# Performance work log

Hardware: AMD Instinct MI355X
Metric: run time of the kernel (lower is better)

The kernel has to match this reference:

```python
import jax, jax.numpy as jnp
import numpy as np
import math

N_HEADS = 8
N_LAYERS = 2
HYPER1 = 0.6
HYPER2 = 0.07


def setup_inputs() -> dict:
    key = jax.random.key(0)
    ks = jax.random.split(key, 32)
    B, S, D, M = 32, 512, 768, 384  # M = mem_dim = D // 2
    rn = lambda k, shape, scale: jax.random.normal(k, shape, jnp.float32) * scale
    sd, sm = 1.0 / math.sqrt(D), 1.0 / math.sqrt(M)
    inp = {
        'gcn_inputs': rn(ks[0], (B, S, D), 1.0),
        'adj_matrix': jax.random.uniform(ks[1], (B, S, S), jnp.float32),
        'attn_mask': jax.random.randint(ks[2], (B, 1, S), 0, 2).astype(jnp.int32),
        's_mask': jax.random.randint(ks[3], (B, S), 0, 2).astype(jnp.int32),
        'a_mask': jax.random.randint(ks[4], (B, S), 0, 2).astype(jnp.int32),
        # MultiHeadAttention: two Linear(d_model, d_model) for q and k
        'Wq': rn(ks[5], (D, D), sd), 'bq': jnp.zeros((D,), jnp.float32),
        'Wk': rn(ks[6], (D, D), sd), 'bk': jnp.zeros((D,), jnp.float32),
        # semW / depW: layer0 D->M, layer1 M->M
        'semW0': rn(ks[7], (D, M), sd), 'semb0': jnp.zeros((M,), jnp.float32),
        'semW1': rn(ks[8], (M, M), sm), 'semb1': jnp.zeros((M,), jnp.float32),
        'depW0': rn(ks[9], (D, M), sd), 'depb0': jnp.zeros((M,), jnp.float32),
        'depW1': rn(ks[10], (M, M), sm), 'depb1': jnp.zeros((M,), jnp.float32),
        # projection head fc1: M->32, fc2: 32->M
        'fc1W': rn(ks[11], (M, 32), sm), 'fc1b': jnp.zeros((32,), jnp.float32),
        'fc2W': rn(ks[12], (32, M), 1.0 / math.sqrt(32)), 'fc2b': jnp.zeros((M,), jnp.float32),
        # fc3: M->M, fc4: D->M
        'fc3W': rn(ks[13], (M, M), sm), 'fc3b': jnp.zeros((M,), jnp.float32),
        'fc4W': rn(ks[14], (D, M), sd), 'fc4b': jnp.zeros((M,), jnp.float32),
    }
    return inp


def _sim(z1, z2):
    # F.normalize(dim=2) then bmm
    n1 = z1 / jnp.maximum(jnp.linalg.norm(z1, axis=2, keepdims=True), 1e-12)
    n2 = z2 / jnp.maximum(jnp.linalg.norm(z2, axis=2, keepdims=True), 1e-12)
    return jnp.einsum('bsd,btd->bst', n1, n2)


def _diag(m):
    return jnp.diagonal(m, axis1=-2, axis2=-1)


def _scope_semi_loss(z1, z2, sm, am):
    f = lambda x: jnp.exp(x / HYPER2)
    a_z1 = z1 * am[..., None]
    m_between = f(_sim(a_z1, z2))
    m_refl = f(_sim(a_z1, z1))
    s_z1 = z1 * sm[..., None]
    s_z2 = z2 * sm[..., None]
    as_refl = f(_sim(a_z1, s_z1))
    as_between = f(_sim(a_z1, s_z2))
    w = _sim(a_z1, s_z2)
    weighted = f(w * _diag(w)[..., None])
    pos = (_diag(as_between)
           + (as_refl.sum(2) - _diag(as_refl))
           + (weighted.sum(2) - _diag(weighted)))
    alle = m_refl.sum(2) + m_between.sum(2) - _diag(m_refl)
    return -jnp.log(pos / alle)


def reference(gcn_inputs, adj_matrix, attn_mask, s_mask, a_mask,
              Wq, bq, Wk, bk,
              semW0, semb0, semW1, semb1,
              depW0, depb0, depW1, depb1,
              fc1W, fc1b, fc2W, fc2b, fc3W, fc3b, fc4W, fc4b):
    B, S, D = gcn_inputs.shape
    h, dk = N_HEADS, D // N_HEADS

    # ---- MultiHeadAttention -> per-head attention adjacency ----
    q = (gcn_inputs @ Wq + bq).reshape(B, S, h, dk).transpose(0, 2, 1, 3)
    k = (gcn_inputs @ Wk + bk).reshape(B, S, h, dk).transpose(0, 2, 1, 3)
    scores = jnp.einsum('bhsd,bhtd->bhst', q, k) / math.sqrt(dk)
    scores = jnp.where(attn_mask[:, None] == 0, -10000.0, scores)  # [B,1,1,S] broadcast
    attn = jax.nn.softmax(scores, axis=-1)  # dropout in eval mode -> identity

    # average heads, zero diagonal, add identity, row-mask by encoder atts
    adj_ag = attn.mean(axis=1)  # [B,S,S]
    eye = jnp.eye(S, dtype=adj_ag.dtype)
    adj_ag = adj_ag * (1.0 - eye) + eye
    atts = attn_mask.astype(adj_ag.dtype)  # text_encoder_atts [B,1,S]
    adj_ag = jnp.swapaxes(atts, 1, 2) * adj_ag

    # ---- gated dual-GCN layers ----
    sem_params = [(semW0, semb0), (semW1, semb1)]
    dep_params = [(depW0, depb0), (depW1, depb1)]
    H_l = gcn_inputs
    I_sem = None
    for l in range(N_LAYERS):
        sW, sb = sem_params[l]
        dW, db = dep_params[l]
        AH_sem = jnp.einsum('bst,btd->bsd', adj_ag, H_l)
        I_sem = AH_sem @ sW + sb
        AH_dep = jnp.einsum('bst,btd->bsd', adj_matrix, H_l)
        I_dep = AH_dep @ dW + db
        g = jax.nn.sigmoid(I_dep)
        I_dep_g = HYPER1 * g
        I_com = (1.0 - I_dep_g) * I_sem + I_dep_g * I_dep
        H_out = jax.nn.relu(I_com @ fc3W + fc3b)
        if l == 0:
            H_l = H_l @ fc4W + fc4b
        g_l = jax.nn.sigmoid(H_l)
        H_l = g_l * H_out + (1.0 - g_l) * H_l

    # ---- projection + symmetric contrastive scope loss ----
    proj = lambda z: jax.nn.elu(z @ fc1W + fc1b) @ fc2W + fc2b
    h1 = proj(H_l)
    h2 = proj(I_sem)
    smf = s_mask.astype(h1.dtype)
    amf = a_mask.astype(h1.dtype)
    l1 = _scope_semi_loss(h1, h2, smf, amf)
    l2 = _scope_semi_loss(h2, h1, smf, amf)
    loss = (l1 + l2) * 0.5
    loss_cl = loss.mean(axis=1, keepdims=True).mean()
    return loss_cl
```

## Files before the change

kernel.cpp:

```cpp
#include <hip/hip_runtime.h>
#include <math.h>


typedef __bf16 bf16x8 __attribute__((ext_vector_type(8)));
typedef __bf16 bf16x4 __attribute__((ext_vector_type(4)));
typedef float f32x4 __attribute__((ext_vector_type(4)));

__device__ __forceinline__ void glds16(const void* g, void* l) {
    __builtin_amdgcn_global_load_lds(
        (const __attribute__((address_space(1))) unsigned*)g,
        (__attribute__((address_space(3))) unsigned*)l, 16, 0, 0);
}

__device__ __forceinline__ float sigf(float x) { return 1.f / (1.f + __expf(-x)); }

__global__ __launch_bounds__(256) void mfma_gemm(
    const __bf16* __restrict__ A, const __bf16* __restrict__ B,
    const float* __restrict__ bias, int bzDiv, int bzStride,
    const __bf16* __restrict__ E,
    float* __restrict__ Cf, __bf16* __restrict__ Cb,
    int K, int lda, int ldb, int ldc, int nMax,
    long sAo, long sAi, long sBo, long sBi, int zInner, long sC, int act)
{
    __shared__ __bf16 As[2][128 * 32];
    __shared__ __bf16 Bs[2][128 * 32];
    int z = blockIdx.z;
    long aBase = (long)(z / zInner) * sAo + (long)(z % zInner) * sAi;
    long bBase = (long)(z / zInner) * sBo + (long)(z % zInner) * sBi;
    long cBase = (long)z * sC;
    int m0 = blockIdx.x * 128, n0 = blockIdx.y * 128;
    int tid = threadIdx.x;
    int wave = tid >> 6, lane = tid & 63;
    int wm = wave >> 1, wn = wave & 1;

    int e0 = tid, e1 = tid + 256;
    const __bf16* Ag0 = A + aBase + (long)(m0 + (e0 >> 2)) * lda + (e0 & 3) * 8;
    const __bf16* Ag1 = A + aBase + (long)(m0 + (e1 >> 2)) * lda + (e1 & 3) * 8;
    const __bf16* Bg0 = B + bBase + (long)(n0 + (e0 >> 2)) * ldb + (e0 & 3) * 8;
    const __bf16* Bg1 = B + bBase + (long)(n0 + (e1 >> 2)) * ldb + (e1 & 3) * 8;

    f32x4 acc[4][4];
#pragma unroll
    for (int i = 0; i < 4; i++)
#pragma unroll
        for (int j = 0; j < 4; j++) acc[i][j] = (f32x4){0.f, 0.f, 0.f, 0.f};

    int arow = wm * 64 + (lane & 15);
    int brow = wn * 64 + (lane & 15);
    int quad = lane >> 4;

    glds16(Ag0, As[0] + e0 * 8); glds16(Ag1, As[0] + e1 * 8);
    glds16(Bg0, Bs[0] + e0 * 8); glds16(Bg1, Bs[0] + e1 * 8);

    int cur = 0;
    for (int k0 = 0; k0 < K; k0 += 32) {
        __syncthreads();
        if (k0 + 32 < K) {
            int nk = k0 + 32, nb = cur ^ 1;
            glds16(Ag0 + nk, As[nb] + e0 * 8); glds16(Ag1 + nk, As[nb] + e1 * 8);
            glds16(Bg0 + nk, Bs[nb] + e0 * 8); glds16(Bg1 + nk, Bs[nb] + e1 * 8);
        }
        const bf16x8* Asv = (const bf16x8*)As[cur];
        const bf16x8* Bsv = (const bf16x8*)Bs[cur];
        bf16x8 af[4], bfr[4];
#pragma unroll
        for (int mi = 0; mi < 4; mi++) af[mi] = Asv[(arow + mi * 16) * 4 + quad];
#pragma unroll
        for (int ni = 0; ni < 4; ni++) bfr[ni] = Bsv[(brow + ni * 16) * 4 + quad];
#pragma unroll
        for (int mi = 0; mi < 4; mi++)
#pragma unroll
            for (int ni = 0; ni < 4; ni++)
                acc[mi][ni] = __builtin_amdgcn_mfma_f32_16x16x32_bf16(
                    af[mi], bfr[ni], acc[mi][ni], 0, 0, 0);
        cur ^= 1;
    }

    int crow = m0 + wm * 64 + (lane >> 4) * 4;
    int ccol = n0 + wn * 64 + (lane & 15);
    const float* biasz = bias ? bias + (z / bzDiv) * bzStride : nullptr;
    float bv[4];
#pragma unroll
    for (int ni = 0; ni < 4; ni++) {
        int col = ccol + ni * 16;
        bv[ni] = (biasz && col < nMax) ? biasz[col] : 0.f;
    }
#pragma unroll
    for (int mi = 0; mi < 4; mi++) {
#pragma unroll
        for (int ni = 0; ni < 4; ni++) {
            int col = ccol + ni * 16;
            if (col >= nMax) continue;
#pragma unroll
            for (int r = 0; r < 4; r++) {
                float v = acc[mi][ni][r] + bv[ni];
                long idx = cBase + (long)(crow + mi * 16 + r) * ldc + col;
                if (act == 1) v = fmaxf(v, 0.f);
                else if (act == 2) v = (v > 0.f) ? v : expm1f(v);
                else if (act == 4) {
                    float e = (float)E[idx];
                    v = fmaxf(v, 0.f);
                    float g = sigf(e);
                    v = g * v + (1.f - g) * e;
                }
                if (Cf) Cf[idx] = v;
                if (Cb) Cb[idx] = (__bf16)v;
            }
        }
    }
}

struct WCast {
    const float* src[10];
    unsigned dstOff[10];
    int R[10], C[10];
    int start[11];
};

__global__ __launch_bounds__(256) void castW_kernel(WCast wc, __bf16* wb)
{
    __shared__ float t[32][33];
    int bid = blockIdx.x;
    int e = 0;
    while (bid >= wc.start[e + 1]) e++;
    int tt = bid - wc.start[e];
    int cT = wc.C[e] >> 5;
    int ty = tt / cT, tx = tt - ty * cT;
    const float* in = wc.src[e];
    __bf16* out = wb + wc.dstOff[e];
    int R = wc.R[e], C = wc.C[e];
    int r0 = ty * 32, c0 = tx * 32;
    int tid = threadIdx.x;
    int r = tid >> 3, c4 = (tid & 7) * 4;
    float4 v = *(const float4*)(in + (long)(r0 + r) * C + c0 + c4);
    t[r][c4] = v.x; t[r][c4 + 1] = v.y; t[r][c4 + 2] = v.z; t[r][c4 + 3] = v.w;
    __syncthreads();
    int c = tid >> 3, r4 = (tid & 7) * 4;
    bf16x4 o;
    o[0] = (__bf16)t[r4 + 0][c]; o[1] = (__bf16)t[r4 + 1][c];
    o[2] = (__bf16)t[r4 + 2][c]; o[3] = (__bf16)t[r4 + 3][c];
    *(bf16x4*)(out + (long)(c0 + c) * R + r0 + r4) = o;
}

__global__ void cast_bf16_kernel(const float* __restrict__ in, __bf16* __restrict__ out, long n4)
{
    long i = (long)blockIdx.x * blockDim.x + threadIdx.x;
    if (i < n4) {
        float4 v = ((const float4*)in)[i];
        bf16x4 o; o[0] = (__bf16)v.x; o[1] = (__bf16)v.y; o[2] = (__bf16)v.z; o[3] = (__bf16)v.w;
        ((bf16x4*)out)[i] = o;
    }
}

__global__ __launch_bounds__(256) void softmax_combine(
    const __bf16* __restrict__ scores, const int* __restrict__ attn_mask,
    __bf16* __restrict__ adj_agb, int b0)
{
    const int S = 512;
    int s = blockIdx.x, bl = blockIdx.y, b = b0 + bl;
    int tid = threadIdx.x;
    const float scale = 0.1020620726159658f;
    int t0 = tid, t1 = tid + 256;
    int cm0 = attn_mask[b * S + t0], cm1 = attn_mask[b * S + t1];
    float vals[8][2], part[8];
#pragma unroll
    for (int h = 0; h < 8; ++h) {
        long rb = ((long)(bl * 8 + h) * S + s) * S;
        float r0 = (float)scores[rb + t0], r1 = (float)scores[rb + t1];
        vals[h][0] = cm0 ? __expf(r0 * scale) : 0.f;
        vals[h][1] = cm1 ? __expf(r1 * scale) : 0.f;
        part[h] = vals[h][0] + vals[h][1];
    }
    __shared__ float red[4][8];
    __shared__ float linv[8];
    int lane = tid & 63, w = tid >> 6;
#pragma unroll
    for (int h = 0; h < 8; ++h) {
        float v = part[h];
        for (int o = 32; o > 0; o >>= 1) v += __shfl_down(v, o);
        if (lane == 0) red[w][h] = v;
    }
    __syncthreads();
    if (tid < 8) {
        float l = red[0][tid] + red[1][tid] + red[2][tid] + red[3][tid];
        linv[tid] = 1.f / fmaxf(l, 1e-30f);
    }
    __syncthreads();
    float rowmask = attn_mask[b * S + s] ? 1.f : 0.f;
    float a0 = 0.f, a1 = 0.f;
#pragma unroll
    for (int h = 0; h < 8; ++h) { a0 += vals[h][0] * linv[h]; a1 += vals[h][1] * linv[h]; }
    a0 *= 0.125f; a1 *= 0.125f;
    if (t0 == s) a0 = 1.f;
    if (t1 == s) a1 = 1.f;
    long ob = ((long)b * S + s) * S;
    adj_agb[ob + t0] = (__bf16)(rowmask * a0);
    adj_agb[ob + t1] = (__bf16)(rowmask * a1);
}

__global__ void gcn_combine2(const __bf16* __restrict__ IsIdb,
                             __bf16* __restrict__ Icomb, long n8)
{
    long i = (long)blockIdx.x * blockDim.x + threadIdx.x;
    if (i >= n8) return;
    bf16x8 sv = ((const bf16x8*)IsIdb)[i];
    bf16x8 dv = ((const bf16x8*)(IsIdb + n8 * 8))[i];
    bf16x8 o;
#pragma unroll
    for (int j = 0; j < 8; j++) {
        float s = (float)sv[j], d = (float)dv[j];
        float g = 0.6f * sigf(d);
        o[j] = (__bf16)((1.f - g) * s + g * d);
    }
    ((bf16x8*)Icomb)[i] = o;
}

__global__ __launch_bounds__(128) void rownorm(__bf16* __restrict__ hb, int Dm)
{
    __bf16* p = hb + (long)blockIdx.x * Dm;
    int tid = threadIdx.x;
    float ss = 0.f;
    for (int i = tid; i < Dm; i += 128) { float v = (float)p[i]; ss += v * v; }
    for (int o = 32; o > 0; o >>= 1) ss += __shfl_down(ss, o);
    __shared__ float sb[2];
    __shared__ float scale;
    if ((tid & 63) == 0) sb[tid >> 6] = ss;
    __syncthreads();
    if (tid == 0) scale = 1.f / fmaxf(sqrtf(sb[0] + sb[1]), 1e-12f);
    __syncthreads();
    for (int i = tid; i < Dm; i += 128) p[i] = (__bf16)((float)p[i] * scale);
}

__global__ __launch_bounds__(256) void loss_kernel(
    const __bf16* __restrict__ G11, const __bf16* __restrict__ G12,
    const __bf16* __restrict__ G22,
    const int* __restrict__ s_mask, const int* __restrict__ a_mask,
    float* __restrict__ lossb)
{
    const int S = 512;
    int s = blockIdx.x, b = blockIdx.y;
    int tid = threadIdx.x;
    if (a_mask[b * S + s] == 0) {
        if (tid == 0) lossb[b * S + s] = 0.f;
        return;
    }
    long base = ((long)b * S + s) * S;
    long cbase = (long)b * S * S + s;
    const float it = 1.f / 0.07f;
    float sms = s_mask[b * S + s] ? 1.f : 0.f;
    float d12 = (float)G12[base + s];
    float w1i = sms * d12 * it, w2i = w1i;
    float p[8];
#pragma unroll
    for (int h = 0; h < 8; h++) p[h] = 0.f;
#pragma unroll
    for (int j = 0; j < 2; j++) {
        int t = tid + j * 256;
        bool smt = s_mask[b * S + t] != 0;
        bool off = (t != s);
        float g11 = (float)G11[base + t], g12 = (float)G12[base + t];
        float g21 = (float)G12[cbase + (long)t * S];
        float g22 = (float)G22[base + t];
        float e11 = __expf(g11 * it), e12 = __expf(g12 * it);
        float e21 = __expf(g21 * it), e22 = __expf(g22 * it);
        p[2] += e11; p[3] += e12; p[6] += e22; p[7] += e21;
        if (off) {
            p[0] += smt ? e11 : 1.f;
            p[4] += smt ? e22 : 1.f;
            p[1] += smt ? __expf(g12 * w1i) : 1.f;
            p[5] += smt ? __expf(g21 * w2i) : 1.f;
        }
    }
    __shared__ float red[4][8];
    int lane = tid & 63, w = tid >> 6;
#pragma unroll
    for (int h = 0; h < 8; h++) {
        float v = p[h];
        for (int o = 32; o > 0; o >>= 1) v += __shfl_down(v, o);
        if (lane == 0) red[w][h] = v;
    }
    __syncthreads();
    if (tid == 0) {
        float r[8];
#pragma unroll
        for (int h = 0; h < 8; h++) r[h] = red[0][h] + red[1][h] + red[2][h] + red[3][h];
        float g11ss = (float)G11[base + s], g22ss = (float)G22[base + s];
        float pos1 = __expf(w1i) + r[0] + r[1];
        float alle1 = r[2] - __expf(g11ss * it) + r[3];
        float pos2 = __expf(w2i) + r[4] + r[5];
        float alle2 = r[6] - __expf(g22ss * it) + r[7];
        lossb[b * S + s] = 0.5f * ((__logf(alle1) - __logf(pos1)) +
                                   (__logf(alle2) - __logf(pos2)));
    }
}

__global__ __launch_bounds__(256) void final_reduce(
    const float* __restrict__ lossb, float* __restrict__ out, int n)
{
    int tid = threadIdx.x;
    float s = 0.f;
    for (int i = tid; i < n; i += 256) s += lossb[i];
    for (int o = 32; o > 0; o >>= 1) s += __shfl_down(s, o);
    __shared__ float sb[4];
    if ((tid & 63) == 0) sb[tid >> 6] = s;
    __syncthreads();
    if (tid == 0) out[0] = (sb[0] + sb[1] + sb[2] + sb[3]) / (float)n;
}

static inline void mg(hipStream_t st, const __bf16* A, const __bf16* B,
                      const float* bias, int bzDiv, int bzStride,
                      const __bf16* E, float* Cf, __bf16* Cb,
                      int M, int Npad, int nMax, int K, int lda, int ldb, int ldc,
                      long sAo, long sAi, long sBo, long sBi, int zInner, long sC, int nz,
                      int act)
{
    dim3 g(M / 128, Npad / 128, nz);
    mfma_gemm<<<g, 256, 0, st>>>(A, B, bias, bzDiv, bzStride, E, Cf, Cb,
                                 K, lda, ldb, ldc, nMax,
                                 sAo, sAi, sBo, sBi, zInner, sC, act);
}

extern "C" void kernel_launch(void* const* d_in, const int* in_sizes, int n_in,
                              void* d_out, int out_size, void* d_ws, size_t ws_size,
                              hipStream_t stream)
{
    const int B = 32, S = 512, D = 768, Mm = 384;
    const int MT = B * S;
    const float* X    = (const float*)d_in[0];
    const float* adjm = (const float*)d_in[1];
    const int* attn_mask = (const int*)d_in[2];
    const int* s_mask    = (const int*)d_in[3];
    const int* a_mask    = (const int*)d_in[4];
    const float* Wq = (const float*)d_in[5],  *bq = (const float*)d_in[6];
    const float* Wk = (const float*)d_in[7],  *bk = (const float*)d_in[8];
    const float* semW0 = (const float*)d_in[9],  *semb0 = (const float*)d_in[10];
    const float* semW1 = (const float*)d_in[11], *semb1 = (const float*)d_in[12];
    const float* depW0 = (const float*)d_in[13], *depb0 = (const float*)d_in[14];
    const float* depW1 = (const float*)d_in[15], *depb1 = (const float*)d_in[16];
    const float* fc1W = (const float*)d_in[17], *fc1b = (const float*)d_in[18];
    const float* fc2W = (const float*)d_in[19], *fc2b = (const float*)d_in[20];
    const float* fc3W = (const float*)d_in[21], *fc3b = (const float*)d_in[22];
    const float* fc4W = (const float*)d_in[23], *fc4b = (const float*)d_in[24];

    char* ws = (char*)d_ws;
    const size_t MB = 1u << 20;
    const size_t KB = 1u << 10;

    __bf16* Xb      = (__bf16*)(ws + 0 * MB);
    __bf16* adj_agb = (__bf16*)(ws + 24 * MB);
    __bf16* adjmb   = (__bf16*)(ws + 40 * MB);
    __bf16* qkb     = (__bf16*)(ws + 56 * MB);
    __bf16* scoreB  = (__bf16*)(ws + 104 * MB);
    __bf16* P64     = (__bf16*)(ws + 56 * MB);
    __bf16* IsIdb   = (__bf16*)(ws + 80 * MB);
    __bf16* Isemb   = IsIdb;
    __bf16* Icomb   = (__bf16*)(ws + 104 * MB);
    __bf16* Hpreb   = (__bf16*)(ws + 116 * MB);
    __bf16* Hb      = (__bf16*)(ws + 128 * MB);
    __bf16* t1b     = (__bf16*)(ws + 0 * MB);
    __bf16* hb12    = (__bf16*)(ws + 140 * MB);
    __bf16* h1b     = hb12;
    __bf16* h2b     = hb12 + (long)MT * Mm;
    __bf16* G11     = (__bf16*)(ws + 24 * MB);
    __bf16* G12     = (__bf16*)(ws + 40 * MB);
    __bf16* G22     = (__bf16*)(ws + 72 * MB);

    char* wreg = ws + 192 * MB;
    __bf16* wb     = (__bf16*)wreg;
    __bf16* WqkT   = (__bf16*)(wreg + 0 * KB);
    __bf16* semW0T = (__bf16*)(wreg + 2304 * KB);
    __bf16* depW0T = (__bf16*)(wreg + 2880 * KB);
    __bf16* fc4WT  = (__bf16*)(wreg + 3456 * KB);
    __bf16* semW1T = (__bf16*)(wreg + 4032 * KB);
    __bf16* depW1T = (__bf16*)(wreg + 4320 * KB);
    __bf16* fc3WT  = (__bf16*)(wreg + 4608 * KB);
    __bf16* fc1WT  = (__bf16*)(wreg + 4896 * KB);
    __bf16* fc2WT  = (__bf16*)(wreg + 4992 * KB);
    float*  bqk    = (float*)(wreg + 5016 * KB);
    float*  sbd0   = (float*)(wreg + 5024 * KB);
    float*  sbd1   = (float*)(wreg + 5028 * KB);
    float*  lossb  = (float*)(wreg + 5036 * KB);

    long nSM = (long)S * Mm, nSS = (long)S * S;
    long nPM = (long)Mm * S;

    cast_bf16_kernel<<<(MT * D / 4 + 255) / 256, 256, 0, stream>>>(X, Xb, (long)MT * D / 4);
    cast_bf16_kernel<<<((long)B * nSS / 4 + 255) / 256, 256, 0, stream>>>(adjm, adjmb, (long)B * nSS / 4);
    {
        WCast wc;
        const float* srcs[10] = {Wq, Wk, semW0, depW0, fc4W, semW1, depW1, fc3W, fc1W, fc2W};
        unsigned offs[10] = {0u, 589824u, 1179648u, 1474560u, 1769472u,
                             2064384u, 2211840u, 2359296u, 2506752u, 2555904u};
        int Rs[10] = {768, 768, 768, 768, 768, 384, 384, 384, 384, 32};
        int Cs[10] = {768, 768, 384, 384, 384, 384, 384, 384, 32, 384};
        int st = 0;
        for (int i = 0; i < 10; i++) {
            wc.src[i] = srcs[i]; wc.dstOff[i] = offs[i];
            wc.R[i] = Rs[i]; wc.C[i] = Cs[i];
            wc.start[i] = st; st += (Rs[i] / 32) * (Cs[i] / 32);
        }
        wc.start[10] = st;
        castW_kernel<<<st, 256, 0, stream>>>(wc, wb);
    }
    hipMemsetAsync(fc1WT + 32 * Mm, 0, (size_t)96 * Mm * 2, stream);
    hipMemcpyAsync(bqk, bq, D * 4, hipMemcpyDeviceToDevice, stream);
    hipMemcpyAsync(bqk + D, bk, D * 4, hipMemcpyDeviceToDevice, stream);
    hipMemcpyAsync(sbd0, semb0, Mm * 4, hipMemcpyDeviceToDevice, stream);
    hipMemcpyAsync(sbd0 + Mm, depb0, Mm * 4, hipMemcpyDeviceToDevice, stream);
    hipMemcpyAsync(sbd1, semb1, Mm * 4, hipMemcpyDeviceToDevice, stream);
    hipMemcpyAsync(sbd1 + Mm, depb1, Mm * 4, hipMemcpyDeviceToDevice, stream);

    mg(stream, Xb, WqkT, bqk, 1, 0, nullptr, nullptr, qkb, MT, 1536, 1536, D,
       D, D, 1536, 0, 0, 0, 0, 1, 0, 1, 0);

    for (int c = 0; c < 2; c++) {
        const __bf16* qc = qkb + (long)c * 16 * S * 1536;
        mg(stream, qc, qc + 768, nullptr, 1, 0, nullptr, nullptr, scoreB, S, S, S, 96,
           1536, 1536, S, (long)S * 1536, 96, (long)S * 1536, 96, 8, nSS, 128, 0);
        softmax_combine<<<dim3(S, 16), 256, 0, stream>>>(scoreB, attn_mask, adj_agb, c * 16);
    }

    long n8 = (long)MT * Mm / 8;
    int cwg = (int)((n8 + 255) / 256);

    mg(stream, semW0T, Xb, nullptr, 1, 0, nullptr, nullptr, P64, Mm, S, S, D,
       D, D, S, (long)Mm * D, 0, 0, (long)S * D, 32, nPM, 64, 0);
    mg(stream, adj_agb, P64, sbd0, 32, Mm, nullptr, nullptr, IsIdb, S, Mm, Mm, S,
       S, S, Mm, 0, nSS, 0, nPM, 64, nSM, 64, 0);
    gcn_combine2<<<cwg, 256, 0, stream>>>(IsIdb, Icomb, n8);
    mg(stream, Xb, fc4WT, fc4b, 1, 0, nullptr, nullptr, Hpreb, MT, Mm, Mm, D,
       D, D, Mm, 0, 0, 0, 0, 1, 0, 1, 0);
    mg(stream, Icomb, fc3WT, fc3b, 1, 0, Hpreb, nullptr, Hb, MT, Mm, Mm, Mm,
       Mm, Mm, Mm, 0, 0, 0, 0, 1, 0, 1, 4);

    mg(stream, semW1T, Hb, nullptr, 1, 0, nullptr, nullptr, P64, Mm, S, S, Mm,
       Mm, Mm, S, (long)Mm * Mm, 0, 0, nSM, 32, nPM, 64, 0);
    mg(stream, adj_agb, P64, sbd1, 32, Mm, nullptr, nullptr, IsIdb, S, Mm, Mm, S,
       S, S, Mm, 0, nSS, 0, nPM, 64, nSM, 64, 0);
    gcn_combine2<<<cwg, 256, 0, stream>>>(IsIdb, Icomb, n8);
    mg(stream, Icomb, fc3WT, fc3b, 1, 0, Hb, nullptr, Hb, MT, Mm, Mm, Mm,
       Mm, Mm, Mm, 0, 0, 0, 0, 1, 0, 1, 4);

    long sAproj = (long)(Isemb - Hb);
    mg(stream, Hb, fc1WT, fc1b, 1, 0, nullptr, nullptr, t1b, MT, 128, 32, Mm,
       Mm, Mm, 32, 0, sAproj, 0, 0, 2, (long)MT * 32, 2, 2);
    mg(stream, t1b, fc2WT, fc2b, 1, 0, nullptr, nullptr, hb12, MT, Mm, Mm, 32,
       32, 32, Mm, 0, (long)MT * 32, 0, 0, 2, (long)MT * Mm, 2, 0);

    rownorm<<<2 * MT, 128, 0, stream>>>(hb12, Mm);

    mg(stream, h1b, h1b, nullptr, 1, 0, nullptr, nullptr, G11, S, S, S, Mm,
       Mm, Mm, S, 0, nSM, 32 * nSM, nSM, 32, nSS, 64, 0);
    mg(stream, h2b, h2b, nullptr, 1, 0, nullptr, nullptr, G22, S, S, S, Mm,
       Mm, Mm, S, 0, nSM, 0, nSM, 32, nSS, 32, 0);

    loss_kernel<<<dim3(S, B), 256, 0, stream>>>(G11, G12, G22, s_mask, a_mask, lossb);
    final_reduce<<<1, 256, 0, stream>>>(lossb, (float*)d_out, MT);
}
```

Before: 793.4 us.

## Fuse fc4 into QK GEMM and gate combine into dep adjacency GEMM

The fc4 projection is folded into the Q/K projection GEMM by widening the weight matrix to 1920 columns, so X is read once and one launch is removed. The fc3 epilogue then reads its residual from a strided slice of that output. The separate gcn_combine2 kernel is removed: the sem and dep adjacency GEMMs are now split, and the dep GEMM applies the sigmoid gate in its epilogue (act 5) against the stored sem result. This saves a full pass over the intermediate, at the cost of a wider QK buffer and two smaller batched GEMM launches instead of one.

```diff
diff --git a/kernel.cpp b/kernel.cpp
--- a/kernel.cpp
+++ b/kernel.cpp
@@ -17,7 +17,7 @@
 __global__ __launch_bounds__(256) void mfma_gemm(
     const __bf16* __restrict__ A, const __bf16* __restrict__ B,
     const float* __restrict__ bias, int bzDiv, int bzStride,
-    const __bf16* __restrict__ E,
+    const __bf16* __restrict__ E, long ldE, long sCE,
     float* __restrict__ Cf, __bf16* __restrict__ Cb,
     int K, int lda, int ldb, int ldc, int nMax,
     long sAo, long sAi, long sBo, long sBi, int zInner, long sC, int act)
@@ -94,14 +94,19 @@
 #pragma unroll
             for (int r = 0; r < 4; r++) {
                 float v = acc[mi][ni][r] + bv[ni];
-                long idx = cBase + (long)(crow + mi * 16 + r) * ldc + col;
+                int row = crow + mi * 16 + r;
+                long idx = cBase + (long)row * ldc + col;
                 if (act == 1) v = fmaxf(v, 0.f);
                 else if (act == 2) v = (v > 0.f) ? v : expm1f(v);
                 else if (act == 4) {
-                    float e = (float)E[idx];
+                    float e = (float)E[(long)z * sCE + (long)row * ldE + col];
                     v = fmaxf(v, 0.f);
                     float g = sigf(e);
                     v = g * v + (1.f - g) * e;
+                } else if (act == 5) {
+                    float s = (float)E[(long)z * sCE + (long)row * ldE + col];
+                    float g = 0.6f * sigf(v);
+                    v = (1.f - g) * s + g * v;
                 }
                 if (Cf) Cf[idx] = v;
                 if (Cb) Cb[idx] = (__bf16)v;
@@ -196,23 +201,6 @@
     long ob = ((long)b * S + s) * S;
     adj_agb[ob + t0] = (__bf16)(rowmask * a0);
     adj_agb[ob + t1] = (__bf16)(rowmask * a1);
-}
-
-__global__ void gcn_combine2(const __bf16* __restrict__ IsIdb,
-                             __bf16* __restrict__ Icomb, long n8)
-{
-    long i = (long)blockIdx.x * blockDim.x + threadIdx.x;
-    if (i >= n8) return;
-    bf16x8 sv = ((const bf16x8*)IsIdb)[i];
-    bf16x8 dv = ((const bf16x8*)(IsIdb + n8 * 8))[i];
-    bf16x8 o;
-#pragma unroll
-    for (int j = 0; j < 8; j++) {
-        float s = (float)sv[j], d = (float)dv[j];
-        float g = 0.6f * sigf(d);
-        o[j] = (__bf16)((1.f - g) * s + g * d);
-    }
-    ((bf16x8*)Icomb)[i] = o;
 }
 
 __global__ __launch_bounds__(128) void rownorm(__bf16* __restrict__ hb, int Dm)
@@ -309,13 +297,14 @@
 
 static inline void mg(hipStream_t st, const __bf16* A, const __bf16* B,
                       const float* bias, int bzDiv, int bzStride,
-                      const __bf16* E, float* Cf, __bf16* Cb,
+                      const __bf16* E, long ldE, long sCE,
+                      float* Cf, __bf16* Cb,
                       int M, int Npad, int nMax, int K, int lda, int ldb, int ldc,
                       long sAo, long sAi, long sBo, long sBi, int zInner, long sC, int nz,
                       int act)
 {
     dim3 g(M / 128, Npad / 128, nz);
-    mfma_gemm<<<g, 256, 0, st>>>(A, B, bias, bzDiv, bzStride, E, Cf, Cb,
+    mfma_gemm<<<g, 256, 0, st>>>(A, B, bias, bzDiv, bzStride, E, ldE, sCE, Cf, Cb,
                                  K, lda, ldb, ldc, nMax,
                                  sAo, sAi, sBo, sBi, zInner, sC, act);
 }
@@ -350,45 +339,45 @@
     __bf16* adj_agb = (__bf16*)(ws + 24 * MB);
     __bf16* adjmb   = (__bf16*)(ws + 40 * MB);
     __bf16* qkb     = (__bf16*)(ws + 56 * MB);
-    __bf16* scoreB  = (__bf16*)(ws + 104 * MB);
-    __bf16* P64     = (__bf16*)(ws + 56 * MB);
-    __bf16* IsIdb   = (__bf16*)(ws + 80 * MB);
+    __bf16* scoreB  = (__bf16*)(ws + 116 * MB);
+    __bf16* P64     = (__bf16*)(ws + 116 * MB);
+    __bf16* IsIdb   = (__bf16*)(ws + 140 * MB);
     __bf16* Isemb   = IsIdb;
-    __bf16* Icomb   = (__bf16*)(ws + 104 * MB);
-    __bf16* Hpreb   = (__bf16*)(ws + 116 * MB);
-    __bf16* Hb      = (__bf16*)(ws + 128 * MB);
-    __bf16* t1b     = (__bf16*)(ws + 0 * MB);
-    __bf16* hb12    = (__bf16*)(ws + 140 * MB);
+    __bf16* Icomb   = (__bf16*)(ws + 152 * MB);
+    __bf16* Hb      = (__bf16*)(ws + 164 * MB);
+    __bf16* t1b     = (__bf16*)(ws + 176 * MB);
+    __bf16* hb12    = (__bf16*)(ws + 0 * MB);
     __bf16* h1b     = hb12;
     __bf16* h2b     = hb12 + (long)MT * Mm;
     __bf16* G11     = (__bf16*)(ws + 24 * MB);
     __bf16* G12     = (__bf16*)(ws + 40 * MB);
-    __bf16* G22     = (__bf16*)(ws + 72 * MB);
+    __bf16* G22     = (__bf16*)(ws + 56 * MB);
 
     char* wreg = ws + 192 * MB;
     __bf16* wb     = (__bf16*)wreg;
     __bf16* WqkT   = (__bf16*)(wreg + 0 * KB);
-    __bf16* semW0T = (__bf16*)(wreg + 2304 * KB);
-    __bf16* depW0T = (__bf16*)(wreg + 2880 * KB);
-    __bf16* fc4WT  = (__bf16*)(wreg + 3456 * KB);
+    __bf16* fc4WT  = (__bf16*)(wreg + 2304 * KB);
+    __bf16* semW0T = (__bf16*)(wreg + 2880 * KB);
+    __bf16* depW0T = (__bf16*)(wreg + 3456 * KB);
     __bf16* semW1T = (__bf16*)(wreg + 4032 * KB);
     __bf16* depW1T = (__bf16*)(wreg + 4320 * KB);
     __bf16* fc3WT  = (__bf16*)(wreg + 4608 * KB);
     __bf16* fc1WT  = (__bf16*)(wreg + 4896 * KB);
     __bf16* fc2WT  = (__bf16*)(wreg + 4992 * KB);
-    float*  bqk    = (float*)(wreg + 5016 * KB);
+    float*  bqkf   = (float*)(wreg + 5016 * KB);
     float*  sbd0   = (float*)(wreg + 5024 * KB);
     float*  sbd1   = (float*)(wreg + 5028 * KB);
     float*  lossb  = (float*)(wreg + 5036 * KB);
 
     long nSM = (long)S * Mm, nSS = (long)S * S;
     long nPM = (long)Mm * S;
+    const int W = 1920;
 
     cast_bf16_kernel<<<(MT * D / 4 + 255) / 256, 256, 0, stream>>>(X, Xb, (long)MT * D / 4);
     cast_bf16_kernel<<<((long)B * nSS / 4 + 255) / 256, 256, 0, stream>>>(adjm, adjmb, (long)B * nSS / 4);
     {
         WCast wc;
-        const float* srcs[10] = {Wq, Wk, semW0, depW0, fc4W, semW1, depW1, fc3W, fc1W, fc2W};
+        const float* srcs[10] = {Wq, Wk, fc4W, semW0, depW0, semW1, depW1, fc3W, fc1W, fc2W};
         unsigned offs[10] = {0u, 589824u, 1179648u, 1474560u, 1769472u,
                              2064384u, 2211840u, 2359296u, 2506752u, 2555904u};
         int Rs[10] = {768, 768, 768, 768, 768, 384, 384, 384, 384, 32};
@@ -403,55 +392,53 @@
         castW_kernel<<<st, 256, 0, stream>>>(wc, wb);
     }
     hipMemsetAsync(fc1WT + 32 * Mm, 0, (size_t)96 * Mm * 2, stream);
-    hipMemcpyAsync(bqk, bq, D * 4, hipMemcpyDeviceToDevice, stream);
-    hipMemcpyAsync(bqk + D, bk, D * 4, hipMemcpyDeviceToDevice, stream);
+    hipMemcpyAsync(bqkf, bq, D * 4, hipMemcpyDeviceToDevice, stream);
+    hipMemcpyAsync(bqkf + D, bk, D * 4, hipMemcpyDeviceToDevice, stream);
+    hipMemcpyAsync(bqkf + 2 * D, fc4b, Mm * 4, hipMemcpyDeviceToDevice, stream);
     hipMemcpyAsync(sbd0, semb0, Mm * 4, hipMemcpyDeviceToDevice, stream);
     hipMemcpyAsync(sbd0 + Mm, depb0, Mm * 4, hipMemcpyDeviceToDevice, stream);
     hipMemcpyAsync(sbd1, semb1, Mm * 4, hipMemcpyDeviceToDevice, stream);
     hipMemcpyAsync(sbd1 + Mm, depb1, Mm * 4, hipMemcpyDeviceToDevice, stream);
 
-    mg(stream, Xb, WqkT, bqk, 1, 0, nullptr, nullptr, qkb, MT, 1536, 1536, D,
-       D, D, 1536, 0, 0, 0, 0, 1, 0, 1, 0);
+    mg(stream, Xb, WqkT, bqkf, 1, 0, nullptr, 0, 0, nullptr, qkb, MT, W, W, D,
+       D, D, W, 0, 0, 0, 0, 1, 0, 1, 0);
 
     for (int c = 0; c < 2; c++) {
-        const __bf16* qc = qkb + (long)c * 16 * S * 1536;
-        mg(stream, qc, qc + 768, nullptr, 1, 0, nullptr, nullptr, scoreB, S, S, S, 96,
-           1536, 1536, S, (long)S * 1536, 96, (long)S * 1536, 96, 8, nSS, 128, 0);
+        const __bf16* qc = qkb + (long)c * 16 * S * W;
+        mg(stream, qc, qc + 768, nullptr, 1, 0, nullptr, 0, 0, nullptr, scoreB, S, S, S, 96,
+           W, W, S, (long)S * W, 96, (long)S * W, 96, 8, nSS, 128, 0);
         softmax_combine<<<dim3(S, 16), 256, 0, stream>>>(scoreB, attn_mask, adj_agb, c * 16);
     }
 
-    long n8 = (long)MT * Mm / 8;
-    int cwg = (int)((n8 + 255) / 256);
-
-    mg(stream, semW0T, Xb, nullptr, 1, 0, nullptr, nullptr, P64, Mm, S, S, D,
+    mg(stream, semW0T, Xb, nullptr, 1, 0, nullptr, 0, 0, nullptr, P64, Mm, S, S, D,
        D, D, S, (long)Mm * D, 0, 0, (long)S * D, 32, nPM, 64, 0);
-    mg(stream, adj_agb, P64, sbd0, 32, Mm, nullptr, nullptr, IsIdb, S, Mm, Mm, S,
-       S, S, Mm, 0, nSS, 0, nPM, 64, nSM, 64, 0);
-    gcn_combine2<<<cwg, 256, 0, stream>>>(IsIdb, Icomb, n8);
-    mg(stream, Xb, fc4WT, fc4b, 1, 0, nullptr, nullptr, Hpreb, MT, Mm, Mm, D,
-       D, D, Mm, 0, 0, 0, 0, 1, 0, 1, 0);
-    mg(stream, Icomb, fc3WT, fc3b, 1, 0, Hpreb, nullptr, Hb, MT, Mm, Mm, Mm,
+    mg(stream, adj_agb, P64, sbd0, 1, 0, nullptr, 0, 0, nullptr, IsIdb, S, Mm, Mm, S,
+       S, S, Mm, 0, nSS, 0, nPM, 32, nSM, 32, 0);
+    mg(stream, adjmb, P64 + 32 * nPM, sbd0 + Mm, 1, 0, IsIdb, Mm, nSM, nullptr, Icomb,
+       S, Mm, Mm, S, S, S, Mm, 0, nSS, 0, nPM, 32, nSM, 32, 5);
+    mg(stream, Icomb, fc3WT, fc3b, 1, 0, qkb + 1536, W, 0, nullptr, Hb, MT, Mm, Mm, Mm,
        Mm, Mm, Mm, 0, 0, 0, 0, 1, 0, 1, 4);
 
-    mg(stream, semW1T, Hb, nullptr, 1, 0, nullptr, nullptr, P64, Mm, S, S, Mm,
+    mg(stream, semW1T, Hb, nullptr, 1, 0, nullptr, 0, 0, nullptr, P64, Mm, S, S, Mm,
        Mm, Mm, S, (long)Mm * Mm, 0, 0, nSM, 32, nPM, 64, 0);
-    mg(stream, adj_agb, P64, sbd1, 32, Mm, nullptr, nullptr, IsIdb, S, Mm, Mm, S,
-       S, S, Mm, 0, nSS, 0, nPM, 64, nSM, 64, 0);
-    gcn_combine2<<<cwg, 256, 0, stream>>>(IsIdb, Icomb, n8);
-    mg(stream, Icomb, fc3WT, fc3b, 1, 0, Hb, nullptr, Hb, MT, Mm, Mm, Mm,
+    mg(stream, adj_agb, P64, sbd1, 1, 0, nullptr, 0, 0, nullptr, IsIdb, S, Mm, Mm, S,
+       S, S, Mm, 0, nSS, 0, nPM, 32, nSM, 32, 0);
+    mg(stream, adjmb, P64 + 32 * nPM, sbd1 + Mm, 1, 0, IsIdb, Mm, nSM, nullptr, Icomb,
+       S, Mm, Mm, S, S, S, Mm, 0, nSS, 0, nPM, 32, nSM, 32, 5);
+    mg(stream, Icomb, fc3WT, fc3b, 1, 0, Hb, Mm, 0, nullptr, Hb, MT, Mm, Mm, Mm,
        Mm, Mm, Mm, 0, 0, 0, 0, 1, 0, 1, 4);
 
     long sAproj = (long)(Isemb - Hb);
-    mg(stream, Hb, fc1WT, fc1b, 1, 0, nullptr, nullptr, t1b, MT, 128, 32, Mm,
+    mg(stream, Hb, fc1WT, fc1b, 1, 0, nullptr, 0, 0, nullptr, t1b, MT, 128, 32, Mm,
        Mm, Mm, 32, 0, sAproj, 0, 0, 2, (long)MT * 32, 2, 2);
-    mg(stream, t1b, fc2WT, fc2b, 1, 0, nullptr, nullptr, hb12, MT, Mm, Mm, 32,
+    mg(stream, t1b, fc2WT, fc2b, 1, 0, nullptr, 0, 0, nullptr, hb12, MT, Mm, Mm, 32,
        32, 32, Mm, 0, (long)MT * 32, 0, 0, 2, (long)MT * Mm, 2, 0);
 
     rownorm<<<2 * MT, 128, 0, stream>>>(hb12, Mm);
 
-    mg(stream, h1b, h1b, nullptr, 1, 0, nullptr, nullptr, G11, S, S, S, Mm,
+    mg(stream, h1b, h1b, nullptr, 1, 0, nullptr, 0, 0, nullptr, G11, S, S, S, Mm,
        Mm, Mm, S, 0, nSM, 32 * nSM, nSM, 32, nSS, 64, 0);
-    mg(stream, h2b, h2b, nullptr, 1, 0, nullptr, nullptr, G22, S, S, S, Mm,
+    mg(stream, h2b, h2b, nullptr, 1, 0, nullptr, 0, 0, nullptr, G22, S, S, S, Mm,
        Mm, Mm, S, 0, nSM, 0, nSM, 32, nSS, 32, 0);
 
     loss_kernel<<<dim3(S, B), 256, 0, stream>>>(G11, G12, G22, s_mask, a_mask, lossb);
```

After: 848.7 us. 1.07x slower.
